# Optimization experiments

Measured on AMD Instinct MI355X. Metric: run time of the kernel, lower is better.

## Reference

```python
import jax, jax.numpy as jnp
import numpy as np

B, N, DIM = 2, 2048, 512
H = 8
DH = DIM // H
ALPHA = 1.0
DELTA = 1.0
EPS = 1e-5


def setup_inputs() -> dict:
    key = jax.random.key(0)
    ks = jax.random.split(key, 5)
    scale = 0.02
    return {
        "z": jax.random.normal(ks[0], (B, N, DIM), dtype=jnp.float32),
        "Wq": jax.random.normal(ks[1], (DIM, DIM), dtype=jnp.float32) * scale,
        "bq": jnp.zeros((DIM,), dtype=jnp.float32),
        "Wk": jax.random.normal(ks[2], (DIM, DIM), dtype=jnp.float32) * scale,
        "bk": jnp.zeros((DIM,), dtype=jnp.float32),
        "Wv": jax.random.normal(ks[3], (DIM, DIM), dtype=jnp.float32) * scale,
        "bv": jnp.zeros((DIM,), dtype=jnp.float32),
        "Wo": jax.random.normal(ks[4], (DIM, DIM), dtype=jnp.float32) * scale,
        "bo": jnp.zeros((DIM,), dtype=jnp.float32),
    }


def _split_heads(x):
    # [B, N, DIM] -> [B, H, N, DH]
    b, n, _ = x.shape
    return x.reshape(b, n, H, DH).transpose(0, 2, 1, 3)


def reference(z, Wq, bq, Wk, bk, Wv, bv, Wo, bo):
    Q = _split_heads(z @ Wq + bq)
    K = _split_heads(z @ Wk + bk)
    V = _split_heads(z @ Wv + bv)

    # QK^T once; reuse for both the score and the squared-distance expansion
    qk = jnp.einsum("bhnd,bhmd->bhnm", Q, K)  # [B,H,N,N]

    # NeuroFocal deviation NF(Q): per-query scalar
    mu_q = Q.mean(axis=-1, keepdims=True)
    var_q = ((Q - mu_q) ** 2).mean(axis=-1, keepdims=True)
    sigma_q = jnp.sqrt(var_q + EPS)
    nf_q = jnp.abs(Q - mu_q).sum(axis=-1, keepdims=True) / (sigma_q + EPS)  # [B,H,N,1]

    # ||Q - K||^2 = |Q|^2 + |K|^2 - 2 QK^T (same math as explicit diff tensor)
    q2 = (Q ** 2).sum(axis=-1)  # [B,H,N]
    k2 = (K ** 2).sum(axis=-1)  # [B,H,N]
    omega = q2[..., :, None] + k2[..., None, :] - 2.0 * qk  # [B,H,N,N]
    omega = omega / (jnp.exp(-DELTA * nf_q) + 1.0)

    logits = qk / jnp.sqrt(jnp.float32(DH)) - ALPHA * omega
    A = jax.nn.softmax(logits, axis=-1)

    out = jnp.einsum("bhnm,bhmd->bhnd", A, V)  # [B,H,N,DH]
    out = out.transpose(0, 2, 1, 3).reshape(z.shape[0], z.shape[1], DIM)
    return out @ Wo + bo
```

## Files before the change

kernel.cpp:

```cpp
#include <hip/hip_runtime.h>
#include <hip/hip_bf16.h>

#define HH 8
#define NNq 2048
#define EPSF 1e-5f
#define LOG2E 1.4426950408889634f

typedef __bf16 bf16x8 __attribute__((ext_vector_type(8)));
typedef float f32x4 __attribute__((ext_vector_type(4)));

typedef const __attribute__((address_space(1))) unsigned int* gas_t;
typedef __attribute__((address_space(3))) unsigned int* las_t;

__device__ __forceinline__ void async16(const void* g, void* l) {
  __builtin_amdgcn_global_load_lds((gas_t)g, (las_t)l, 16, 0, 0);
}
__device__ __forceinline__ void async4(const void* g, void* l) {
  __builtin_amdgcn_global_load_lds((gas_t)g, (las_t)l, 4, 0, 0);
}

__device__ __forceinline__ unsigned short f2bf(float f) {
  union { float f; unsigned int u; } a;
  a.f = f;
  unsigned int r = a.u + 0x7fffu + ((a.u >> 16) & 1u);
  return (unsigned short)(r >> 16);
}

__device__ __forceinline__ int swzk(int row, int k) {
  return (k & ~63) | ((((k >> 3) ^ row) & 7) << 3) | (k & 7);
}

__global__ __launch_bounds__(256) void prep_kernel(
    const float* __restrict__ z, const float* __restrict__ W0,
    const float* __restrict__ W1, const float* __restrict__ W2,
    const float* __restrict__ W3, unsigned short* __restrict__ zb,
    unsigned short* __restrict__ Wt, unsigned int* __restrict__ k2max) {
  __shared__ float Tl[64][68];
  const int t = threadIdx.x;
  const int bx = blockIdx.x;
  if (bx < 1024) {
    const int i = (bx * 256 + t) * 8;
    const int row = i >> 9, k = i & 511;
    const float4 a = *(const float4*)&z[i];
    const float4 b = *(const float4*)&z[i + 4];
    union { unsigned short us[8]; uint4 v; } o;
    o.us[0] = f2bf(a.x); o.us[1] = f2bf(a.y); o.us[2] = f2bf(a.z); o.us[3] = f2bf(a.w);
    o.us[4] = f2bf(b.x); o.us[5] = f2bf(b.y); o.us[6] = f2bf(b.z); o.us[7] = f2bf(b.w);
    *(uint4*)&zb[(row << 9) | swzk(row, k)] = o.v;
  } else if (bx < 1280) {
    const int idx0 = bx - 1024;
    const int wsel = idx0 >> 6, rem = idx0 & 63;
    const int k0 = (rem >> 3) * 64, n0 = (rem & 7) * 64;
    const float* W = (wsel == 0) ? W0 : (wsel == 1) ? W1 : (wsel == 2) ? W2 : W3;
    unsigned short* dst = Wt + (size_t)wsel * 262144;
#pragma unroll
    for (int i = 0; i < 4; ++i) {
      const int idx = t + 256 * i;
      const int row = idx >> 4, cq = (idx & 15) * 4;
      *(float4*)&Tl[row][cq] = *(const float4*)&W[(size_t)(k0 + row) * 512 + n0 + cq];
    }
    __syncthreads();
#pragma unroll
    for (int i = 0; i < 4; ++i) {
      const int idx = t + 256 * i;
      const int nr = idx >> 4, kq = (idx & 15) * 4;
      ushort4 o;
      o.x = f2bf(Tl[kq + 0][nr]);
      o.y = f2bf(Tl[kq + 1][nr]);
      o.z = f2bf(Tl[kq + 2][nr]);
      o.w = f2bf(Tl[kq + 3][nr]);
      const int n = n0 + nr;
      *(ushort4*)&dst[(size_t)n * 512 + swzk(n, k0 + kq)] = o;
    }
  } else {
    k2max[t] = 0u;
  }
}

__global__ __launch_bounds__(256) void gemm_qkv(
    const unsigned short* __restrict__ A, const unsigned short* __restrict__ Wt3,
    const float* __restrict__ bq, const float* __restrict__ bk,
    const float* __restrict__ bvv, unsigned short* __restrict__ Qb,
    unsigned short* __restrict__ Ksw, unsigned short* __restrict__ Vsw,
    float* __restrict__ c1a, float* __restrict__ dva, float* __restrict__ k2a,
    float* __restrict__ q2a, unsigned int* __restrict__ k2max) {
  __shared__ __align__(16) unsigned short S[24576];
  __shared__ float wmax[4];

  const int which = blockIdx.z;
  const unsigned short* Wt = Wt3 + (size_t)which * 262144;
  const float* bias = (which == 0) ? bq : (which == 1) ? bk : bvv;

  const int t = threadIdx.x;
  const int w = t >> 6, lane = t & 63, ln = lane & 15, quad = lane >> 4;
  const int r0 = blockIdx.x * 128, h = blockIdx.y;
  const int c0 = h * 64;
  const int b = r0 >> 11, n0 = r0 & 2047;
  const int bh = b * HH + h;

  f32x4 acc[2][4];
#pragma unroll
  for (int rf = 0; rf < 2; ++rf)
#pragma unroll
    for (int nt = 0; nt < 4; ++nt) acc[rf][nt] = (f32x4)(0.0f);

  const int lr = lane >> 4, lc = (lane & 15) * 8;

  for (int k0 = 0; k0 < 512; k0 += 128) {
#pragma unroll
    for (int i = 0; i < 8; ++i)
      async16(A + (size_t)(r0 + w * 32 + i * 4 + lr) * 512 + k0 + lc,
              S + (w * 32 + i * 4) * 128);
#pragma unroll
    for (int i = 0; i < 4; ++i)
      async16(Wt + (size_t)(c0 + w * 16 + i * 4 + lr) * 512 + k0 + lc,
              S + 16384 + (w * 16 + i * 4) * 128);
    __syncthreads();
#pragma unroll
    for (int kk = 0; kk < 128; kk += 32) {
      const int cp = (kk >> 3) + quad;
      const int cs = ((cp & 8) | ((cp ^ (ln & 7)) & 7)) * 8;
      bf16x8 af[2];
#pragma unroll
      for (int rf = 0; rf < 2; ++rf)
        af[rf] = *(const bf16x8*)&S[(w * 32 + rf * 16 + ln) * 128 + cs];
#pragma unroll
      for (int nt = 0; nt < 4; ++nt) {
        const bf16x8 bf = *(const bf16x8*)&S[16384 + (nt * 16 + ln) * 128 + cs];
#pragma unroll
        for (int rf = 0; rf < 2; ++rf)
          acc[rf][nt] = __builtin_amdgcn_mfma_f32_16x16x32_bf16(af[rf], bf, acc[rf][nt], 0, 0, 0);
      }
    }
    __syncthreads();
  }

  float x[2][4][4];
#pragma unroll
  for (int nt = 0; nt < 4; ++nt) {
    const float bv = bias[c0 + nt * 16 + ln];
#pragma unroll
    for (int rf = 0; rf < 2; ++rf)
#pragma unroll
      for (int r = 0; r < 4; ++r) x[rf][nt][r] = acc[rf][nt][r] + bv;
  }

  if (which == 0) {
#pragma unroll
    for (int rf = 0; rf < 2; ++rf)
#pragma unroll
      for (int r = 0; r < 4; ++r) {
        float s1 = x[rf][0][r] + x[rf][1][r] + x[rf][2][r] + x[rf][3][r];
#pragma unroll
        for (int off = 1; off < 16; off <<= 1) s1 += __shfl_xor(s1, off, 64);
        const float mu = s1 * (1.0f / 64.0f);
        float s2 = 0.0f, sa = 0.0f;
#pragma unroll
        for (int nt = 0; nt < 4; ++nt) {
          const float dx = x[rf][nt][r] - mu;
          s2 += dx * dx;
          sa += fabsf(dx);
        }
#pragma unroll
        for (int off = 1; off < 16; off <<= 1) {
          s2 += __shfl_xor(s2, off, 64);
          sa += __shfl_xor(sa, off, 64);
        }
        if (ln == 0) {
          const float sigma = sqrtf(s2 * (1.0f / 64.0f) + EPSF);
          const float nf = sa / (sigma + EPSF);
          const float dInv = 1.0f / (__expf(-nf) + 1.0f);
          const int row = bh * NNq + n0 + w * 32 + rf * 16 + quad * 4 + r;
          c1a[row] = (0.125f + 2.0f * dInv) * LOG2E;
          dva[row] = dInv * LOG2E;
          q2a[row] = s2 + 64.0f * mu * mu;
        }
      }
#pragma unroll
    for (int rf = 0; rf < 2; ++rf)
#pragma unroll
      for (int nt = 0; nt < 4; ++nt)
#pragma unroll
        for (int r = 0; r < 4; ++r)
          S[(w * 32 + rf * 16 + quad * 4 + r) * 72 + nt * 16 + ln] = f2bf(x[rf][nt][r]);
    __syncthreads();
#pragma unroll
    for (int i = 0; i < 4; ++i) {
      const int idx = t + 256 * i;
      const int q = idx >> 3, c = idx & 7;
      *(uint4*)&Qb[((size_t)bh * NNq + n0 + q) * 64 + c * 8] =
          *(const uint4*)&S[q * 72 + c * 8];
    }
  } else if (which == 1) {
    float mx = 0.0f;
#pragma unroll
    for (int rf = 0; rf < 2; ++rf)
#pragma unroll
      for (int r = 0; r < 4; ++r) {
        float s2 = 0.0f;
#pragma unroll
        for (int nt = 0; nt < 4; ++nt) s2 += x[rf][nt][r] * x[rf][nt][r];
#pragma unroll
        for (int off = 1; off < 16; off <<= 1) s2 += __shfl_xor(s2, off, 64);
        if (ln == 0) k2a[bh * NNq + n0 + w * 32 + rf * 16 + quad * 4 + r] = s2;
        mx = fmaxf(mx, s2);
      }
#pragma unroll
    for (int off = 16; off < 64; off <<= 1) mx = fmaxf(mx, __shfl_xor(mx, off, 64));
    if (lane == 0) wmax[w] = mx;
#pragma unroll
    for (int rf = 0; rf < 2; ++rf)
#pragma unroll
      for (int nt = 0; nt < 4; ++nt) {
        const int c = nt * 2 + (ln >> 3);
#pragma unroll
        for (int r = 0; r < 4; ++r) {
          const int key = w * 32 + rf * 16 + quad * 4 + r;
          const int klo = key & 63;
          S[(key >> 6) * 4096 + klo * 64 + ((c ^ (klo & 7)) * 8) + (ln & 7)] =
              f2bf(x[rf][nt][r]);
        }
      }
    __syncthreads();
    if (t == 0) {
      const float m = fmaxf(fmaxf(wmax[0], wmax[1]), fmaxf(wmax[2], wmax[3]));
      atomicMax(&k2max[bh * 16], __float_as_uint(m));
    }
    unsigned short* dst = Ksw + ((size_t)bh * 32 + (n0 >> 6)) * 4096;
#pragma unroll
    for (int i = 0; i < 4; ++i) {
      const int idx = t + 256 * i;
      *(uint4*)&dst[idx * 8] = *(const uint4*)&S[idx * 8];
    }
  } else {
#pragma unroll
    for (int rf = 0; rf < 2; ++rf)
#pragma unroll
      for (int nt = 0; nt < 4; ++nt) {
        const int d = nt * 16 + ln;
#pragma unroll
        for (int r = 0; r < 4; ++r) {
          const int key = w * 32 + rf * 16 + quad * 4 + r;
          const int klo = key & 63;
          S[d * 128 + (key >> 6) * 64 + (((klo >> 3) ^ (d & 7)) * 8) + (klo & 7)] =
              f2bf(x[rf][nt][r]);
        }
      }
    __syncthreads();
    unsigned short* dst = Vsw + ((size_t)bh * 32 + (n0 >> 6)) * 4096;
#pragma unroll
    for (int i = 0; i < 4; ++i) {
      const int g = t + 256 * i;
      const int tile = g >> 9, d = (g >> 3) & 63, j8 = (g & 7) * 8;
      *(uint4*)&dst[tile * 4096 + d * 64 + j8] =
          *(const uint4*)&S[d * 128 + tile * 64 + j8];
    }
  }
}

__global__ __launch_bounds__(512) void attn_kernel(
    const unsigned short* __restrict__ Qb, const unsigned short* __restrict__ Ksw,
    const unsigned short* __restrict__ Vsw, const float* __restrict__ c1a,
    const float* __restrict__ dva, const float* __restrict__ k2a,
    const float* __restrict__ q2a, const unsigned int* __restrict__ k2maxu,
    unsigned short* __restrict__ attnb) {
  __shared__ __align__(16) char smem[59392];

  const int t = threadIdx.x;
  const int w8 = t >> 6, lane = t & 63, ln = lane & 15, quad = lane >> 4;
  const int half = w8 >> 2, wl = w8 & 3;
  const int qt = blockIdx.x, bh = blockIdx.y;
  const int b = bh >> 3, h = bh & 7;
  const int q0 = qt * 64;
  const int rowbase = bh * NNq;

  unsigned short* Kt = (unsigned short*)(smem + half * 16384);
  unsigned short* Vt = (unsigned short*)(smem + half * 16384 + 8192);
  unsigned short* Ps = (unsigned short*)(smem + 32768 + half * 9216);
  float* k2h = (float*)(smem + 51200 + half * 4096);

  const float* k2g = k2a + rowbase + half * 1024;
#pragma unroll
  for (int i = 0; i < 4; ++i)
    async4(k2g + wl * 256 + i * 64 + lane, k2h + wl * 256 + i * 64);

  const int qg = q0 + wl * 16 + ln;
  const unsigned short* qrow = Qb + ((size_t)rowbase + qg) * 64;
  const bf16x8 aq0 = *(const bf16x8*)(qrow + quad * 8);
  const bf16x8 aq1 = *(const bf16x8*)(qrow + 32 + quad * 8);

  const float k2m = __uint_as_float(k2maxu[bh * 16]);
  const float c1q = c1a[rowbase + qg];
  const float dvq = dva[rowbase + qg];
  const float Mqq = c1q * sqrtf(q2a[rowbase + qg] * k2m);
  float L = 0.0f;
  f32x4 O[4];
#pragma unroll
  for (int nt = 0; nt < 4; ++nt) O[nt] = (f32x4)(0.0f);

  const unsigned short* Kg = Ksw + (size_t)bh * 32 * 4096;
  const unsigned short* Vg = Vsw + (size_t)bh * 32 * 4096;
  const int sw = quad ^ (ln & 7);
  const int sw1 = (4 + quad) ^ (ln & 7);

  for (int kt = 0; kt < 16; ++kt) {
    {
      const size_t tb = (size_t)(half * 16 + kt) * 4096 + wl * 1024;
      async16(Kg + tb + lane * 8, Kt + wl * 1024);
      async16(Kg + tb + 512 + lane * 8, Kt + wl * 1024 + 512);
      async16(Vg + tb + lane * 8, Vt + wl * 1024);
      async16(Vg + tb + 512 + lane * 8, Vt + wl * 1024 + 512);
    }
    __syncthreads();

    f32x4 s[4];
#pragma unroll
    for (int nt = 0; nt < 4; ++nt) {
      const unsigned short* kb = Kt + (nt * 16 + ln) * 64;
      const bf16x8 b0 = *(const bf16x8*)(kb + sw * 8);
      const bf16x8 b1 = *(const bf16x8*)(kb + sw1 * 8);
      f32x4 a = (f32x4)(0.0f);
      a = __builtin_amdgcn_mfma_f32_16x16x32_bf16(b0, aq0, a, 0, 0, 0);
      a = __builtin_amdgcn_mfma_f32_16x16x32_bf16(b1, aq1, a, 0, 0, 0);
      s[nt] = a;
    }

#pragma unroll
    for (int nt = 0; nt < 4; ++nt) {
      const f32x4 k2v = *(const f32x4*)&k2h[kt * 64 + nt * 16 + quad * 4];
      const float p0 = __builtin_amdgcn_exp2f(c1q * s[nt][0] - dvq * k2v[0] - Mqq);
      const float p1 = __builtin_amdgcn_exp2f(c1q * s[nt][1] - dvq * k2v[1] - Mqq);
      const float p2 = __builtin_amdgcn_exp2f(c1q * s[nt][2] - dvq * k2v[2] - Mqq);
      const float p3 = __builtin_amdgcn_exp2f(c1q * s[nt][3] - dvq * k2v[3] - Mqq);
      L += (p0 + p1) + (p2 + p3);
      union { __hip_bfloat162 h; unsigned int u; } c01, c23;
      c01.h = __float22bfloat162_rn(make_float2(p0, p1));
      c23.h = __float22bfloat162_rn(make_float2(p2, p3));
      uint2 pu; pu.x = c01.u; pu.y = c23.u;
      *(uint2*)&Ps[(wl * 16 + ln) * 72 + nt * 16 + quad * 4] = pu;
    }
    const unsigned short* pr = Ps + (wl * 16 + ln) * 72;
    const bf16x8 pa0 = *(const bf16x8*)(pr + quad * 8);
    const bf16x8 pa1 = *(const bf16x8*)(pr + 32 + quad * 8);

#pragma unroll
    for (int nt = 0; nt < 4; ++nt) {
      const unsigned short* vb = Vt + (nt * 16 + ln) * 64;
      const bf16x8 vb0 = *(const bf16x8*)(vb + sw * 8);
      const bf16x8 vb1 = *(const bf16x8*)(vb + sw1 * 8);
      O[nt] = __builtin_amdgcn_mfma_f32_16x16x32_bf16(pa0, vb0, O[nt], 0, 0, 0);
      O[nt] = __builtin_amdgcn_mfma_f32_16x16x32_bf16(pa1, vb1, O[nt], 0, 0, 0);
    }
    __syncthreads();
  }

  L += __shfl_xor(L, 16, 64);
  L += __shfl_xor(L, 32, 64);

  float* Ost = (float*)(smem + half * 16384);
  float* Lst = (float*)(smem + 32768 + half * 9216);
#pragma unroll
  for (int nt = 0; nt < 4; ++nt)
#pragma unroll
    for (int r = 0; r < 4; ++r)
      Ost[(wl * 16 + quad * 4 + r) * 64 + nt * 16 + ln] = O[nt][r];
  if (quad == 0) Lst[wl * 16 + ln] = L;
  __syncthreads();

  const float* O0 = (const float*)smem;
  const float* O1 = (const float*)(smem + 16384);
  const float* L0 = (const float*)(smem + 32768);
  const float* L1 = (const float*)(smem + 32768 + 9216);
  const int q = t >> 3, c8 = (t & 7) * 8;
  const float inv = 1.0f / (L0[q] + L1[q]);
  const int base = q * 64 + c8;
  float4 a0 = *(const float4*)&O0[base];
  float4 a1 = *(const float4*)&O0[base + 4];
  const float4 b0 = *(const float4*)&O1[base];
  const float4 b1 = *(const float4*)&O1[base + 4];
  union { unsigned short us[8]; uint4 v; } ov;
  ov.us[0] = f2bf((a0.x + b0.x) * inv);
  ov.us[1] = f2bf((a0.y + b0.y) * inv);
  ov.us[2] = f2bf((a0.z + b0.z) * inv);
  ov.us[3] = f2bf((a0.w + b0.w) * inv);
  ov.us[4] = f2bf((a1.x + b1.x) * inv);
  ov.us[5] = f2bf((a1.y + b1.y) * inv);
  ov.us[6] = f2bf((a1.z + b1.z) * inv);
  ov.us[7] = f2bf((a1.w + b1.w) * inv);
  const int nrow = q0 + q;
  *(uint4*)&attnb[((size_t)(b * NNq + nrow)) * 512 + swzk(nrow, h * 64 + c8)] = ov.v;
}

__global__ __launch_bounds__(256) void gemm_out(
    const unsigned short* __restrict__ A, const unsigned short* __restrict__ Wt,
    const float* __restrict__ bias, float* __restrict__ of) {
  __shared__ __align__(16) char sbuf[32768];
  unsigned short* S = (unsigned short*)sbuf;
  float (*Tl)[68] = (float(*)[68])sbuf;

  const int t = threadIdx.x;
  const int w = t >> 6, lane = t & 63, ln = lane & 15, quad = lane >> 4;
  const int r0 = blockIdx.x * 64, c0 = blockIdx.y * 64;
  const int lr = lane >> 4, lc = (lane & 15) * 8;

  f32x4 acc[4];
#pragma unroll
  for (int nt = 0; nt < 4; ++nt) acc[nt] = (f32x4)(0.0f);

  for (int k0 = 0; k0 < 512; k0 += 128) {
#pragma unroll
    for (int i = 0; i < 4; ++i) {
      async16(A + (size_t)(r0 + w * 16 + i * 4 + lr) * 512 + k0 + lc,
              S + (w * 16 + i * 4) * 128);
      async16(Wt + (size_t)(c0 + w * 16 + i * 4 + lr) * 512 + k0 + lc,
              S + 8192 + (w * 16 + i * 4) * 128);
    }
    __syncthreads();
#pragma unroll
    for (int kk = 0; kk < 128; kk += 32) {
      const int cp = (kk >> 3) + quad;
      const int cs = ((cp & 8) | ((cp ^ (ln & 7)) & 7)) * 8;
      const bf16x8 af = *(const bf16x8*)&S[(w * 16 + ln) * 128 + cs];
#pragma unroll
      for (int nt = 0; nt < 4; ++nt) {
        const bf16x8 bf = *(const bf16x8*)&S[8192 + (nt * 16 + ln) * 128 + cs];
        acc[nt] = __builtin_amdgcn_mfma_f32_16x16x32_bf16(af, bf, acc[nt], 0, 0, 0);
      }
    }
    __syncthreads();
  }
#pragma unroll
  for (int nt = 0; nt < 4; ++nt) {
    const float bv = bias[c0 + nt * 16 + ln];
#pragma unroll
    for (int r = 0; r < 4; ++r)
      Tl[w * 16 + quad * 4 + r][nt * 16 + ln] = acc[nt][r] + bv;
  }
  __syncthreads();
#pragma unroll
  for (int i = 0; i < 4; ++i) {
    const int idx = t + 256 * i;
    const int row = idx >> 4, c4 = (idx & 15) * 4;
    *(float4*)&of[(size_t)(r0 + row) * 512 + c0 + c4] = *(const float4*)&Tl[row][c4];
  }
}

extern "C" void kernel_launch(void* const* d_in, const int* in_sizes, int n_in,
                              void* d_out, int out_size, void* d_ws,
                              size_t ws_size, hipStream_t stream) {
  const float* z = (const float*)d_in[0];
  const float* Wq = (const float*)d_in[1];
  const float* bq = (const float*)d_in[2];
  const float* Wk = (const float*)d_in[3];
  const float* bk = (const float*)d_in[4];
  const float* Wv = (const float*)d_in[5];
  const float* bv = (const float*)d_in[6];
  const float* Wo = (const float*)d_in[7];
  const float* bo = (const float*)d_in[8];
  float* out = (float*)d_out;

  char* ws = (char*)d_ws;
  unsigned short* zb = (unsigned short*)(ws);
  unsigned short* Wt = (unsigned short*)(ws + 4194304);
  unsigned short* Qb = (unsigned short*)(ws + 6291456);
  unsigned short* Ksw = (unsigned short*)(ws + 10485760);
  unsigned short* Vsw = (unsigned short*)(ws + 14680064);
  float* c1 = (float*)(ws + 18874368);
  float* dv = (float*)(ws + 19005440);
  float* k2 = (float*)(ws + 19136512);
  float* q2 = (float*)(ws + 19267584);
  unsigned short* attnb = (unsigned short*)(ws + 19398656);
  unsigned int* k2max = (unsigned int*)(ws + 23592960);

  hipLaunchKernelGGL(prep_kernel, dim3(1281), dim3(256), 0, stream, z, Wq, Wk,
                     Wv, Wo, zb, Wt, k2max);
  hipLaunchKernelGGL(gemm_qkv, dim3(32, 8, 3), dim3(256), 0, stream, zb, Wt,
                     bq, bk, bv, Qb, Ksw, Vsw, c1, dv, k2, q2, k2max);
  hipLaunchKernelGGL(attn_kernel, dim3(32, 16), dim3(512), 0, stream, Qb, Ksw,
                     Vsw, c1, dv, k2, q2, k2max, attnb);
  hipLaunchKernelGGL(gemm_out, dim3(64, 8), dim3(256), 0, stream, attnb,
                     Wt + 786432, bo, out);
}
```

Baseline: 135.3 us.

## Split attention over key chunks with 32x32 MFMA and separate combine kernel

The attention kernel now splits each query tile's keys into four chunks across a third grid dimension, giving 2048 blocks of 256 threads instead of 512 blocks of 512. Each block writes unnormalized partial O and L to a workspace, and a new combine kernel sums the partials, normalizes and writes bf16 output. The inner loop also moves from 16x16x32 to 32x32x16 MFMA tiles, with a 2x2 wave split over queries and keys. This is meant to raise occupancy and parallelism on a small problem, at the cost of an extra launch and fp32 partial traffic through global memory (about 32 MB).

```diff
diff --git a/kernel.cpp b/kernel.cpp
--- a/kernel.cpp
+++ b/kernel.cpp
@@ -8,6 +8,7 @@
 
 typedef __bf16 bf16x8 __attribute__((ext_vector_type(8)));
 typedef float f32x4 __attribute__((ext_vector_type(4)));
+typedef float f32x16 __attribute__((ext_vector_type(16)));
 
 typedef const __attribute__((address_space(1))) unsigned int* gas_t;
 typedef __attribute__((address_space(3))) unsigned int* las_t;
@@ -258,137 +259,171 @@
   }
 }
 
-__global__ __launch_bounds__(512) void attn_kernel(
+__global__ __launch_bounds__(256) void attn_kernel(
     const unsigned short* __restrict__ Qb, const unsigned short* __restrict__ Ksw,
     const unsigned short* __restrict__ Vsw, const float* __restrict__ c1a,
     const float* __restrict__ dva, const float* __restrict__ k2a,
     const float* __restrict__ q2a, const unsigned int* __restrict__ k2maxu,
-    unsigned short* __restrict__ attnb) {
-  __shared__ __align__(16) char smem[59392];
+    float* __restrict__ Opart, float* __restrict__ Lpart) {
+  __shared__ __align__(16) char smem[28672];
+  unsigned short* Kt = (unsigned short*)smem;
+  unsigned short* Vt = (unsigned short*)(smem + 8192);
+  float* k2h = (float*)(smem + 26624);
 
   const int t = threadIdx.x;
-  const int w8 = t >> 6, lane = t & 63, ln = lane & 15, quad = lane >> 4;
-  const int half = w8 >> 2, wl = w8 & 3;
-  const int qt = blockIdx.x, bh = blockIdx.y;
-  const int b = bh >> 3, h = bh & 7;
+  const int w4 = t >> 6, lane = t & 63, lq = lane & 31, lh = lane >> 5;
+  const int qi = w4 & 1, ki = w4 >> 1;
+  const int qt = blockIdx.x, bh = blockIdx.y, ks = blockIdx.z;
   const int q0 = qt * 64;
   const int rowbase = bh * NNq;
-
-  unsigned short* Kt = (unsigned short*)(smem + half * 16384);
-  unsigned short* Vt = (unsigned short*)(smem + half * 16384 + 8192);
-  unsigned short* Ps = (unsigned short*)(smem + 32768 + half * 9216);
-  float* k2h = (float*)(smem + 51200 + half * 4096);
-
-  const float* k2g = k2a + rowbase + half * 1024;
-#pragma unroll
-  for (int i = 0; i < 4; ++i)
-    async4(k2g + wl * 256 + i * 64 + lane, k2h + wl * 256 + i * 64);
-
-  const int qg = q0 + wl * 16 + ln;
+  const int pb = (qt * 16 + bh) * 4 + ks;
+
+  unsigned short* Ps = (unsigned short*)(smem + 16384 + w4 * 2560);
+
+  const float* k2g = k2a + rowbase + ks * 512;
+  async4(k2g + (w4 * 2 + 0) * 64 + lane, k2h + (w4 * 2 + 0) * 64);
+  async4(k2g + (w4 * 2 + 1) * 64 + lane, k2h + (w4 * 2 + 1) * 64);
+
+  const int qg = q0 + qi * 32 + lq;
   const unsigned short* qrow = Qb + ((size_t)rowbase + qg) * 64;
-  const bf16x8 aq0 = *(const bf16x8*)(qrow + quad * 8);
-  const bf16x8 aq1 = *(const bf16x8*)(qrow + 32 + quad * 8);
+  bf16x8 bq[4];
+#pragma unroll
+  for (int T = 0; T < 4; ++T) bq[T] = *(const bf16x8*)(qrow + T * 16 + lh * 8);
 
   const float k2m = __uint_as_float(k2maxu[bh * 16]);
   const float c1q = c1a[rowbase + qg];
   const float dvq = dva[rowbase + qg];
   const float Mqq = c1q * sqrtf(q2a[rowbase + qg] * k2m);
   float L = 0.0f;
-  f32x4 O[4];
-#pragma unroll
-  for (int nt = 0; nt < 4; ++nt) O[nt] = (f32x4)(0.0f);
-
-  const unsigned short* Kg = Ksw + (size_t)bh * 32 * 4096;
-  const unsigned short* Vg = Vsw + (size_t)bh * 32 * 4096;
-  const int sw = quad ^ (ln & 7);
-  const int sw1 = (4 + quad) ^ (ln & 7);
-
-  for (int kt = 0; kt < 16; ++kt) {
+  f32x16 O[2];
+  O[0] = (f32x16)(0.0f);
+  O[1] = (f32x16)(0.0f);
+
+  const unsigned short* Kg = Ksw + ((size_t)bh * 32 + ks * 8) * 4096;
+  const unsigned short* Vg = Vsw + ((size_t)bh * 32 + ks * 8) * 4096;
+  const int krow = ki * 32 + lq;
+
+  for (int kt = 0; kt < 8; ++kt) {
     {
-      const size_t tb = (size_t)(half * 16 + kt) * 4096 + wl * 1024;
-      async16(Kg + tb + lane * 8, Kt + wl * 1024);
-      async16(Kg + tb + 512 + lane * 8, Kt + wl * 1024 + 512);
-      async16(Vg + tb + lane * 8, Vt + wl * 1024);
-      async16(Vg + tb + 512 + lane * 8, Vt + wl * 1024 + 512);
-    }
-    __syncthreads();
-
-    f32x4 s[4];
-#pragma unroll
-    for (int nt = 0; nt < 4; ++nt) {
-      const unsigned short* kb = Kt + (nt * 16 + ln) * 64;
-      const bf16x8 b0 = *(const bf16x8*)(kb + sw * 8);
-      const bf16x8 b1 = *(const bf16x8*)(kb + sw1 * 8);
-      f32x4 a = (f32x4)(0.0f);
-      a = __builtin_amdgcn_mfma_f32_16x16x32_bf16(b0, aq0, a, 0, 0, 0);
-      a = __builtin_amdgcn_mfma_f32_16x16x32_bf16(b1, aq1, a, 0, 0, 0);
-      s[nt] = a;
-    }
-
-#pragma unroll
-    for (int nt = 0; nt < 4; ++nt) {
-      const f32x4 k2v = *(const f32x4*)&k2h[kt * 64 + nt * 16 + quad * 4];
-      const float p0 = __builtin_amdgcn_exp2f(c1q * s[nt][0] - dvq * k2v[0] - Mqq);
-      const float p1 = __builtin_amdgcn_exp2f(c1q * s[nt][1] - dvq * k2v[1] - Mqq);
-      const float p2 = __builtin_amdgcn_exp2f(c1q * s[nt][2] - dvq * k2v[2] - Mqq);
-      const float p3 = __builtin_amdgcn_exp2f(c1q * s[nt][3] - dvq * k2v[3] - Mqq);
+      const size_t tb = (size_t)kt * 4096 + w4 * 1024;
+      async16(Kg + tb + lane * 8, Kt + w4 * 1024);
+      async16(Kg + tb + 512 + lane * 8, Kt + w4 * 1024 + 512);
+      async16(Vg + tb + lane * 8, Vt + w4 * 1024);
+      async16(Vg + tb + 512 + lane * 8, Vt + w4 * 1024 + 512);
+    }
+    __syncthreads();
+
+    f32x16 s = (f32x16)(0.0f);
+    const unsigned short* kb = Kt + krow * 64;
+#pragma unroll
+    for (int T = 0; T < 4; ++T) {
+      const int chunk = (T * 2 + lh) ^ (krow & 7);
+      const bf16x8 ak = *(const bf16x8*)(kb + chunk * 8);
+      s = __builtin_amdgcn_mfma_f32_32x32x16_bf16(ak, bq[T], s, 0, 0, 0);
+    }
+
+#pragma unroll
+    for (int rq = 0; rq < 4; ++rq) {
+      const int kb4 = 4 * lh + 8 * rq;
+      const f32x4 k2v = *(const f32x4*)&k2h[kt * 64 + ki * 32 + kb4];
+      const float p0 = __builtin_amdgcn_exp2f(c1q * s[rq * 4 + 0] - dvq * k2v[0] - Mqq);
+      const float p1 = __builtin_amdgcn_exp2f(c1q * s[rq * 4 + 1] - dvq * k2v[1] - Mqq);
+      const float p2 = __builtin_amdgcn_exp2f(c1q * s[rq * 4 + 2] - dvq * k2v[2] - Mqq);
+      const float p3 = __builtin_amdgcn_exp2f(c1q * s[rq * 4 + 3] - dvq * k2v[3] - Mqq);
       L += (p0 + p1) + (p2 + p3);
       union { __hip_bfloat162 h; unsigned int u; } c01, c23;
       c01.h = __float22bfloat162_rn(make_float2(p0, p1));
       c23.h = __float22bfloat162_rn(make_float2(p2, p3));
       uint2 pu; pu.x = c01.u; pu.y = c23.u;
-      *(uint2*)&Ps[(wl * 16 + ln) * 72 + nt * 16 + quad * 4] = pu;
-    }
-    const unsigned short* pr = Ps + (wl * 16 + ln) * 72;
-    const bf16x8 pa0 = *(const bf16x8*)(pr + quad * 8);
-    const bf16x8 pa1 = *(const bf16x8*)(pr + 32 + quad * 8);
-
-#pragma unroll
-    for (int nt = 0; nt < 4; ++nt) {
-      const unsigned short* vb = Vt + (nt * 16 + ln) * 64;
-      const bf16x8 vb0 = *(const bf16x8*)(vb + sw * 8);
-      const bf16x8 vb1 = *(const bf16x8*)(vb + sw1 * 8);
-      O[nt] = __builtin_amdgcn_mfma_f32_16x16x32_bf16(pa0, vb0, O[nt], 0, 0, 0);
-      O[nt] = __builtin_amdgcn_mfma_f32_16x16x32_bf16(pa1, vb1, O[nt], 0, 0, 0);
-    }
-    __syncthreads();
-  }
-
-  L += __shfl_xor(L, 16, 64);
+      *(uint2*)&Ps[lq * 40 + kb4] = pu;
+    }
+
+    bf16x8 pa[2];
+#pragma unroll
+    for (int T2 = 0; T2 < 2; ++T2)
+      pa[T2] = *(const bf16x8*)&Ps[lq * 40 + T2 * 16 + lh * 8];
+#pragma unroll
+    for (int dt = 0; dt < 2; ++dt) {
+      const int dcol = dt * 32 + lq;
+      const unsigned short* vb = Vt + dcol * 64;
+#pragma unroll
+      for (int T2 = 0; T2 < 2; ++T2) {
+        const int chunk = (ki * 4 + T2 * 2 + lh) ^ (dcol & 7);
+        const bf16x8 bv = *(const bf16x8*)(vb + chunk * 8);
+        O[dt] = __builtin_amdgcn_mfma_f32_32x32x16_bf16(pa[T2], bv, O[dt], 0, 0, 0);
+      }
+    }
+    __syncthreads();
+  }
+
   L += __shfl_xor(L, 32, 64);
 
-  float* Ost = (float*)(smem + half * 16384);
-  float* Lst = (float*)(smem + 32768 + half * 9216);
-#pragma unroll
-  for (int nt = 0; nt < 4; ++nt)
-#pragma unroll
-    for (int r = 0; r < 4; ++r)
-      Ost[(wl * 16 + quad * 4 + r) * 64 + nt * 16 + ln] = O[nt][r];
-  if (quad == 0) Lst[wl * 16 + ln] = L;
+  float* Ost = (float*)smem;
+  float* Lst = (float*)(smem + 16384);
+  if (ki == 0) {
+#pragma unroll
+    for (int dt = 0; dt < 2; ++dt)
+#pragma unroll
+      for (int r = 0; r < 16; ++r) {
+        const int qrow2 = qi * 32 + (r & 3) + 8 * (r >> 2) + 4 * lh;
+        Ost[qrow2 * 64 + dt * 32 + lq] = O[dt][r];
+      }
+    if (lane < 32) Lst[qi * 32 + lq] = L;
+  }
   __syncthreads();
-
-  const float* O0 = (const float*)smem;
-  const float* O1 = (const float*)(smem + 16384);
-  const float* L0 = (const float*)(smem + 32768);
-  const float* L1 = (const float*)(smem + 32768 + 9216);
-  const int q = t >> 3, c8 = (t & 7) * 8;
-  const float inv = 1.0f / (L0[q] + L1[q]);
-  const int base = q * 64 + c8;
-  float4 a0 = *(const float4*)&O0[base];
-  float4 a1 = *(const float4*)&O0[base + 4];
-  const float4 b0 = *(const float4*)&O1[base];
-  const float4 b1 = *(const float4*)&O1[base + 4];
-  union { unsigned short us[8]; uint4 v; } ov;
-  ov.us[0] = f2bf((a0.x + b0.x) * inv);
-  ov.us[1] = f2bf((a0.y + b0.y) * inv);
-  ov.us[2] = f2bf((a0.z + b0.z) * inv);
-  ov.us[3] = f2bf((a0.w + b0.w) * inv);
-  ov.us[4] = f2bf((a1.x + b1.x) * inv);
-  ov.us[5] = f2bf((a1.y + b1.y) * inv);
-  ov.us[6] = f2bf((a1.z + b1.z) * inv);
-  ov.us[7] = f2bf((a1.w + b1.w) * inv);
-  const int nrow = q0 + q;
-  *(uint4*)&attnb[((size_t)(b * NNq + nrow)) * 512 + swzk(nrow, h * 64 + c8)] = ov.v;
+  if (ki == 1) {
+#pragma unroll
+    for (int dt = 0; dt < 2; ++dt)
+#pragma unroll
+      for (int r = 0; r < 16; ++r) {
+        const int qrow2 = qi * 32 + (r & 3) + 8 * (r >> 2) + 4 * lh;
+        Ost[qrow2 * 64 + dt * 32 + lq] += O[dt][r];
+      }
+    if (lane < 32) Lst[qi * 32 + lq] += L;
+  }
+  __syncthreads();
+#pragma unroll
+  for (int i = 0; i < 4; ++i) {
+    const int f4 = t + i * 256;
+    *(float4*)&Opart[(size_t)pb * 4096 + f4 * 4] = *(const float4*)&Ost[f4 * 4];
+  }
+  if (t < 64) Lpart[pb * 64 + t] = Lst[t];
+}
+
+__global__ __launch_bounds__(256) void attn_combine(
+    const float* __restrict__ Opart, const float* __restrict__ Lpart,
+    unsigned short* __restrict__ attnb) {
+  const int t = threadIdx.x;
+  const int qt = blockIdx.x, bh = blockIdx.y;
+  const int b = bh >> 3, h = bh & 7;
+  const int q = t >> 2, dseg = (t & 3) * 16;
+  const int pbase = (qt * 16 + bh) * 4;
+
+  float Ls = 0.0f;
+#pragma unroll
+  for (int ks = 0; ks < 4; ++ks) Ls += Lpart[(pbase + ks) * 64 + q];
+  const float inv = 1.0f / Ls;
+
+  float acc[16];
+#pragma unroll
+  for (int j = 0; j < 16; ++j) acc[j] = 0.0f;
+#pragma unroll
+  for (int ks = 0; ks < 4; ++ks) {
+    const float* src = Opart + (size_t)(pbase + ks) * 4096 + q * 64 + dseg;
+#pragma unroll
+    for (int i = 0; i < 4; ++i) {
+      const float4 v = *(const float4*)&src[i * 4];
+      acc[i * 4 + 0] += v.x; acc[i * 4 + 1] += v.y;
+      acc[i * 4 + 2] += v.z; acc[i * 4 + 3] += v.w;
+    }
+  }
+  union { unsigned short us[16]; uint4 v[2]; } ov;
+#pragma unroll
+  for (int j = 0; j < 16; ++j) ov.us[j] = f2bf(acc[j] * inv);
+  const int n = qt * 64 + q;
+  unsigned short* dst = attnb + ((size_t)(b * NNq + n)) * 512;
+  *(uint4*)&dst[swzk(n, h * 64 + dseg)] = ov.v[0];
+  *(uint4*)&dst[swzk(n, h * 64 + dseg + 8)] = ov.v[1];
 }
 
 __global__ __launch_bounds__(256) void gemm_out(
@@ -471,13 +506,17 @@
   float* q2 = (float*)(ws + 19267584);
   unsigned short* attnb = (unsigned short*)(ws + 19398656);
   unsigned int* k2max = (unsigned int*)(ws + 23592960);
+  float* Opart = (float*)(ws + 23593984);
+  float* Lpart = (float*)(ws + 57148416);
 
   hipLaunchKernelGGL(prep_kernel, dim3(1281), dim3(256), 0, stream, z, Wq, Wk,
                      Wv, Wo, zb, Wt, k2max);
   hipLaunchKernelGGL(gemm_qkv, dim3(32, 8, 3), dim3(256), 0, stream, zb, Wt,
                      bq, bk, bv, Qb, Ksw, Vsw, c1, dv, k2, q2, k2max);
-  hipLaunchKernelGGL(attn_kernel, dim3(32, 16), dim3(512), 0, stream, Qb, Ksw,
-                     Vsw, c1, dv, k2, q2, k2max, attnb);
+  hipLaunchKernelGGL(attn_kernel, dim3(32, 16, 4), dim3(256), 0, stream, Qb,
+                     Ksw, Vsw, c1, dv, k2, q2, k2max, Opart, Lpart);
+  hipLaunchKernelGGL(attn_combine, dim3(32, 16), dim3(256), 0, stream, Opart,
+                     Lpart, attnb);
   hipLaunchKernelGGL(gemm_out, dim3(64, 8), dim3(256), 0, stream, attnb,
                      Wt + 786432, bo, out);
 }
```

New measurement: 147.1 us. 1.09x slower.

## Shrink GEMM tiles for more blocks and compute softmax row sums via MFMA

Applied to the files above, without the earlier changes.

The QKV projection tile drops from 128 to 64 rows and the output projection tile from 64 to 32 columns, doubling the grid of each kernel to fill more compute units on this small problem. The per-lane scalar accumulation of the softmax denominator in attention is replaced by two extra MFMAs against a ones vector, which also drops the cross-lane shuffles. The trade-offs are less operand reuse per block, more redundant loads of A and W, and a row sum that is now taken over bf16-rounded probabilities rather than fp32 ones.

```diff
diff --git a/kernel.cpp b/kernel.cpp
--- a/kernel.cpp
+++ b/kernel.cpp
@@ -84,7 +84,7 @@
     unsigned short* __restrict__ Ksw, unsigned short* __restrict__ Vsw,
     float* __restrict__ c1a, float* __restrict__ dva, float* __restrict__ k2a,
     float* __restrict__ q2a, unsigned int* __restrict__ k2max) {
-  __shared__ __align__(16) unsigned short S[24576];
+  __shared__ __align__(16) unsigned short S[16384];
   __shared__ float wmax[4];
 
   const int which = blockIdx.z;
@@ -93,99 +93,86 @@
 
   const int t = threadIdx.x;
   const int w = t >> 6, lane = t & 63, ln = lane & 15, quad = lane >> 4;
-  const int r0 = blockIdx.x * 128, h = blockIdx.y;
+  const int r0 = blockIdx.x * 64, h = blockIdx.y;
   const int c0 = h * 64;
   const int b = r0 >> 11, n0 = r0 & 2047;
   const int bh = b * HH + h;
 
-  f32x4 acc[2][4];
-#pragma unroll
-  for (int rf = 0; rf < 2; ++rf)
-#pragma unroll
-    for (int nt = 0; nt < 4; ++nt) acc[rf][nt] = (f32x4)(0.0f);
+  f32x4 acc[4];
+#pragma unroll
+  for (int nt = 0; nt < 4; ++nt) acc[nt] = (f32x4)(0.0f);
 
   const int lr = lane >> 4, lc = (lane & 15) * 8;
 
   for (int k0 = 0; k0 < 512; k0 += 128) {
 #pragma unroll
-    for (int i = 0; i < 8; ++i)
-      async16(A + (size_t)(r0 + w * 32 + i * 4 + lr) * 512 + k0 + lc,
-              S + (w * 32 + i * 4) * 128);
-#pragma unroll
-    for (int i = 0; i < 4; ++i)
+    for (int i = 0; i < 4; ++i) {
+      async16(A + (size_t)(r0 + w * 16 + i * 4 + lr) * 512 + k0 + lc,
+              S + (w * 16 + i * 4) * 128);
       async16(Wt + (size_t)(c0 + w * 16 + i * 4 + lr) * 512 + k0 + lc,
-              S + 16384 + (w * 16 + i * 4) * 128);
+              S + 8192 + (w * 16 + i * 4) * 128);
+    }
     __syncthreads();
 #pragma unroll
     for (int kk = 0; kk < 128; kk += 32) {
       const int cp = (kk >> 3) + quad;
       const int cs = ((cp & 8) | ((cp ^ (ln & 7)) & 7)) * 8;
-      bf16x8 af[2];
-#pragma unroll
-      for (int rf = 0; rf < 2; ++rf)
-        af[rf] = *(const bf16x8*)&S[(w * 32 + rf * 16 + ln) * 128 + cs];
+      const bf16x8 af = *(const bf16x8*)&S[(w * 16 + ln) * 128 + cs];
 #pragma unroll
       for (int nt = 0; nt < 4; ++nt) {
-        const bf16x8 bf = *(const bf16x8*)&S[16384 + (nt * 16 + ln) * 128 + cs];
-#pragma unroll
-        for (int rf = 0; rf < 2; ++rf)
-          acc[rf][nt] = __builtin_amdgcn_mfma_f32_16x16x32_bf16(af[rf], bf, acc[rf][nt], 0, 0, 0);
-      }
-    }
-    __syncthreads();
-  }
-
-  float x[2][4][4];
+        const bf16x8 bf = *(const bf16x8*)&S[8192 + (nt * 16 + ln) * 128 + cs];
+        acc[nt] = __builtin_amdgcn_mfma_f32_16x16x32_bf16(af, bf, acc[nt], 0, 0, 0);
+      }
+    }
+    __syncthreads();
+  }
+
+  float x[4][4];
 #pragma unroll
   for (int nt = 0; nt < 4; ++nt) {
     const float bv = bias[c0 + nt * 16 + ln];
 #pragma unroll
-    for (int rf = 0; rf < 2; ++rf)
-#pragma unroll
-      for (int r = 0; r < 4; ++r) x[rf][nt][r] = acc[rf][nt][r] + bv;
-  }
+    for (int r = 0; r < 4; ++r) x[nt][r] = acc[nt][r] + bv;
+  }
+  const int rowl = w * 16 + quad * 4;
 
   if (which == 0) {
 #pragma unroll
-    for (int rf = 0; rf < 2; ++rf)
-#pragma unroll
-      for (int r = 0; r < 4; ++r) {
-        float s1 = x[rf][0][r] + x[rf][1][r] + x[rf][2][r] + x[rf][3][r];
-#pragma unroll
-        for (int off = 1; off < 16; off <<= 1) s1 += __shfl_xor(s1, off, 64);
-        const float mu = s1 * (1.0f / 64.0f);
-        float s2 = 0.0f, sa = 0.0f;
-#pragma unroll
-        for (int nt = 0; nt < 4; ++nt) {
-          const float dx = x[rf][nt][r] - mu;
-          s2 += dx * dx;
-          sa += fabsf(dx);
-        }
-#pragma unroll
-        for (int off = 1; off < 16; off <<= 1) {
-          s2 += __shfl_xor(s2, off, 64);
-          sa += __shfl_xor(sa, off, 64);
-        }
-        if (ln == 0) {
-          const float sigma = sqrtf(s2 * (1.0f / 64.0f) + EPSF);
-          const float nf = sa / (sigma + EPSF);
-          const float dInv = 1.0f / (__expf(-nf) + 1.0f);
-          const int row = bh * NNq + n0 + w * 32 + rf * 16 + quad * 4 + r;
-          c1a[row] = (0.125f + 2.0f * dInv) * LOG2E;
-          dva[row] = dInv * LOG2E;
-          q2a[row] = s2 + 64.0f * mu * mu;
-        }
-      }
-#pragma unroll
-    for (int rf = 0; rf < 2; ++rf)
-#pragma unroll
-      for (int nt = 0; nt < 4; ++nt)
-#pragma unroll
-        for (int r = 0; r < 4; ++r)
-          S[(w * 32 + rf * 16 + quad * 4 + r) * 72 + nt * 16 + ln] = f2bf(x[rf][nt][r]);
-    __syncthreads();
-#pragma unroll
-    for (int i = 0; i < 4; ++i) {
+    for (int r = 0; r < 4; ++r) {
+      float s1 = x[0][r] + x[1][r] + x[2][r] + x[3][r];
+#pragma unroll
+      for (int off = 1; off < 16; off <<= 1) s1 += __shfl_xor(s1, off, 64);
+      const float mu = s1 * (1.0f / 64.0f);
+      float s2 = 0.0f, sa = 0.0f;
+#pragma unroll
+      for (int nt = 0; nt < 4; ++nt) {
+        const float dx = x[nt][r] - mu;
+        s2 += dx * dx;
+        sa += fabsf(dx);
+      }
+#pragma unroll
+      for (int off = 1; off < 16; off <<= 1) {
+        s2 += __shfl_xor(s2, off, 64);
+        sa += __shfl_xor(sa, off, 64);
+      }
+      if (ln == 0) {
+        const float sigma = sqrtf(s2 * (1.0f / 64.0f) + EPSF);
+        const float nf = sa / (sigma + EPSF);
+        const float dInv = 1.0f / (__expf(-nf) + 1.0f);
+        const int row = bh * NNq + n0 + rowl + r;
+        c1a[row] = (0.125f + 2.0f * dInv) * LOG2E;
+        dva[row] = dInv * LOG2E;
+        q2a[row] = s2 + 64.0f * mu * mu;
+      }
+    }
+#pragma unroll
+    for (int nt = 0; nt < 4; ++nt)
+#pragma unroll
+      for (int r = 0; r < 4; ++r)
+        S[(rowl + r) * 72 + nt * 16 + ln] = f2bf(x[nt][r]);
+    __syncthreads();
+#pragma unroll
+    for (int i = 0; i < 2; ++i) {
       const int idx = t + 256 * i;
       const int q = idx >> 3, c = idx & 7;
       *(uint4*)&Qb[((size_t)bh * NNq + n0 + q) * 64 + c * 8] =
@@ -194,33 +181,27 @@
   } else if (which == 1) {
     float mx = 0.0f;
 #pragma unroll
-    for (int rf = 0; rf < 2; ++rf)
-#pragma unroll
-      for (int r = 0; r < 4; ++r) {
-        float s2 = 0.0f;
-#pragma unroll
-        for (int nt = 0; nt < 4; ++nt) s2 += x[rf][nt][r] * x[rf][nt][r];
-#pragma unroll
-        for (int off = 1; off < 16; off <<= 1) s2 += __shfl_xor(s2, off, 64);
-        if (ln == 0) k2a[bh * NNq + n0 + w * 32 + rf * 16 + quad * 4 + r] = s2;
-        mx = fmaxf(mx, s2);
-      }
+    for (int r = 0; r < 4; ++r) {
+      float s2 = 0.0f;
+#pragma unroll
+      for (int nt = 0; nt < 4; ++nt) s2 += x[nt][r] * x[nt][r];
+#pragma unroll
+      for (int off = 1; off < 16; off <<= 1) s2 += __shfl_xor(s2, off, 64);
+      if (ln == 0) k2a[bh * NNq + n0 + rowl + r] = s2;
+      mx = fmaxf(mx, s2);
+    }
 #pragma unroll
     for (int off = 16; off < 64; off <<= 1) mx = fmaxf(mx, __shfl_xor(mx, off, 64));
     if (lane == 0) wmax[w] = mx;
 #pragma unroll
-    for (int rf = 0; rf < 2; ++rf)
-#pragma unroll
-      for (int nt = 0; nt < 4; ++nt) {
-        const int c = nt * 2 + (ln >> 3);
-#pragma unroll
-        for (int r = 0; r < 4; ++r) {
-          const int key = w * 32 + rf * 16 + quad * 4 + r;
-          const int klo = key & 63;
-          S[(key >> 6) * 4096 + klo * 64 + ((c ^ (klo & 7)) * 8) + (ln & 7)] =
-              f2bf(x[rf][nt][r]);
-        }
-      }
+    for (int nt = 0; nt < 4; ++nt) {
+      const int c = nt * 2 + (ln >> 3);
+#pragma unroll
+      for (int r = 0; r < 4; ++r) {
+        const int key = rowl + r;
+        S[key * 64 + ((c ^ (key & 7)) * 8) + (ln & 7)] = f2bf(x[nt][r]);
+      }
+    }
     __syncthreads();
     if (t == 0) {
       const float m = fmaxf(fmaxf(wmax[0], wmax[1]), fmaxf(wmax[2], wmax[3]));
@@ -228,32 +209,26 @@
     }
     unsigned short* dst = Ksw + ((size_t)bh * 32 + (n0 >> 6)) * 4096;
 #pragma unroll
-    for (int i = 0; i < 4; ++i) {
+    for (int i = 0; i < 2; ++i) {
       const int idx = t + 256 * i;
       *(uint4*)&dst[idx * 8] = *(const uint4*)&S[idx * 8];
     }
   } else {
 #pragma unroll
-    for (int rf = 0; rf < 2; ++rf)
-#pragma unroll
-      for (int nt = 0; nt < 4; ++nt) {
-        const int d = nt * 16 + ln;
-#pragma unroll
-        for (int r = 0; r < 4; ++r) {
-          const int key = w * 32 + rf * 16 + quad * 4 + r;
-          const int klo = key & 63;
-          S[d * 128 + (key >> 6) * 64 + (((klo >> 3) ^ (d & 7)) * 8) + (klo & 7)] =
-              f2bf(x[rf][nt][r]);
-        }
-      }
+    for (int nt = 0; nt < 4; ++nt) {
+      const int d = nt * 16 + ln;
+#pragma unroll
+      for (int r = 0; r < 4; ++r) {
+        const int key = rowl + r;
+        S[d * 64 + (((key >> 3) ^ (d & 7)) * 8) + (key & 7)] = f2bf(x[nt][r]);
+      }
+    }
     __syncthreads();
     unsigned short* dst = Vsw + ((size_t)bh * 32 + (n0 >> 6)) * 4096;
 #pragma unroll
-    for (int i = 0; i < 4; ++i) {
-      const int g = t + 256 * i;
-      const int tile = g >> 9, d = (g >> 3) & 63, j8 = (g & 7) * 8;
-      *(uint4*)&dst[tile * 4096 + d * 64 + j8] =
-          *(const uint4*)&S[d * 128 + tile * 64 + j8];
+    for (int i = 0; i < 2; ++i) {
+      const int idx = t + 256 * i;
+      *(uint4*)&dst[idx * 8] = *(const uint4*)&S[idx * 8];
     }
   }
 }
@@ -293,7 +268,11 @@
   const float c1q = c1a[rowbase + qg];
   const float dvq = dva[rowbase + qg];
   const float Mqq = c1q * sqrtf(q2a[rowbase + qg] * k2m);
-  float L = 0.0f;
+
+  const __bf16 onev = (__bf16)1.0f;
+  const bf16x8 ones = {onev, onev, onev, onev, onev, onev, onev, onev};
+
+  f32x4 Lacc = (f32x4)(0.0f);
   f32x4 O[4];
 #pragma unroll
   for (int nt = 0; nt < 4; ++nt) O[nt] = (f32x4)(0.0f);
@@ -332,7 +311,6 @@
       const float p1 = __builtin_amdgcn_exp2f(c1q * s[nt][1] - dvq * k2v[1] - Mqq);
       const float p2 = __builtin_amdgcn_exp2f(c1q * s[nt][2] - dvq * k2v[2] - Mqq);
       const float p3 = __builtin_amdgcn_exp2f(c1q * s[nt][3] - dvq * k2v[3] - Mqq);
-      L += (p0 + p1) + (p2 + p3);
       union { __hip_bfloat162 h; unsigned int u; } c01, c23;
       c01.h = __float22bfloat162_rn(make_float2(p0, p1));
       c23.h = __float22bfloat162_rn(make_float2(p2, p3));
@@ -342,6 +320,9 @@
     const unsigned short* pr = Ps + (wl * 16 + ln) * 72;
     const bf16x8 pa0 = *(const bf16x8*)(pr + quad * 8);
     const bf16x8 pa1 = *(const bf16x8*)(pr + 32 + quad * 8);
+
+    Lacc = __builtin_amdgcn_mfma_f32_16x16x32_bf16(pa0, ones, Lacc, 0, 0, 0);
+    Lacc = __builtin_amdgcn_mfma_f32_16x16x32_bf16(pa1, ones, Lacc, 0, 0, 0);
 
 #pragma unroll
     for (int nt = 0; nt < 4; ++nt) {
@@ -354,9 +335,6 @@
     __syncthreads();
   }
 
-  L += __shfl_xor(L, 16, 64);
-  L += __shfl_xor(L, 32, 64);
-
   float* Ost = (float*)(smem + half * 16384);
   float* Lst = (float*)(smem + 32768 + half * 9216);
 #pragma unroll
@@ -364,7 +342,10 @@
 #pragma unroll
     for (int r = 0; r < 4; ++r)
       Ost[(wl * 16 + quad * 4 + r) * 64 + nt * 16 + ln] = O[nt][r];
-  if (quad == 0) Lst[wl * 16 + ln] = L;
+  if (ln == 0) {
+#pragma unroll
+    for (int r = 0; r < 4; ++r) Lst[wl * 16 + quad * 4 + r] = Lacc[r];
+  }
   __syncthreads();
 
   const float* O0 = (const float*)smem;
@@ -394,27 +375,28 @@
 __global__ __launch_bounds__(256) void gemm_out(
     const unsigned short* __restrict__ A, const unsigned short* __restrict__ Wt,
     const float* __restrict__ bias, float* __restrict__ of) {
-  __shared__ __align__(16) char sbuf[32768];
+  __shared__ __align__(16) char sbuf[24576];
   unsigned short* S = (unsigned short*)sbuf;
-  float (*Tl)[68] = (float(*)[68])sbuf;
+  float (*Tl)[36] = (float(*)[36])sbuf;
 
   const int t = threadIdx.x;
   const int w = t >> 6, lane = t & 63, ln = lane & 15, quad = lane >> 4;
-  const int r0 = blockIdx.x * 64, c0 = blockIdx.y * 64;
+  const int r0 = blockIdx.x * 64, c0 = blockIdx.y * 32;
   const int lr = lane >> 4, lc = (lane & 15) * 8;
 
-  f32x4 acc[4];
-#pragma unroll
-  for (int nt = 0; nt < 4; ++nt) acc[nt] = (f32x4)(0.0f);
+  f32x4 acc[2];
+#pragma unroll
+  for (int nt = 0; nt < 2; ++nt) acc[nt] = (f32x4)(0.0f);
 
   for (int k0 = 0; k0 < 512; k0 += 128) {
 #pragma unroll
-    for (int i = 0; i < 4; ++i) {
+    for (int i = 0; i < 4; ++i)
       async16(A + (size_t)(r0 + w * 16 + i * 4 + lr) * 512 + k0 + lc,
               S + (w * 16 + i * 4) * 128);
-      async16(Wt + (size_t)(c0 + w * 16 + i * 4 + lr) * 512 + k0 + lc,
-              S + 8192 + (w * 16 + i * 4) * 128);
-    }
+#pragma unroll
+    for (int i = 0; i < 2; ++i)
+      async16(Wt + (size_t)(c0 + w * 8 + i * 4 + lr) * 512 + k0 + lc,
+              S + 8192 + (w * 8 + i * 4) * 128);
     __syncthreads();
 #pragma unroll
     for (int kk = 0; kk < 128; kk += 32) {
@@ -422,7 +404,7 @@
       const int cs = ((cp & 8) | ((cp ^ (ln & 7)) & 7)) * 8;
       const bf16x8 af = *(const bf16x8*)&S[(w * 16 + ln) * 128 + cs];
 #pragma unroll
-      for (int nt = 0; nt < 4; ++nt) {
+      for (int nt = 0; nt < 2; ++nt) {
         const bf16x8 bf = *(const bf16x8*)&S[8192 + (nt * 16 + ln) * 128 + cs];
         acc[nt] = __builtin_amdgcn_mfma_f32_16x16x32_bf16(af, bf, acc[nt], 0, 0, 0);
       }
@@ -430,7 +412,7 @@
     __syncthreads();
   }
 #pragma unroll
-  for (int nt = 0; nt < 4; ++nt) {
+  for (int nt = 0; nt < 2; ++nt) {
     const float bv = bias[c0 + nt * 16 + ln];
 #pragma unroll
     for (int r = 0; r < 4; ++r)
@@ -438,9 +420,9 @@
   }
   __syncthreads();
 #pragma unroll
-  for (int i = 0; i < 4; ++i) {
+  for (int i = 0; i < 2; ++i) {
     const int idx = t + 256 * i;
-    const int row = idx >> 4, c4 = (idx & 15) * 4;
+    const int row = idx >> 3, c4 = (idx & 7) * 4;
     *(float4*)&of[(size_t)(r0 + row) * 512 + c0 + c4] = *(const float4*)&Tl[row][c4];
   }
 }
@@ -474,10 +456,10 @@
 
   hipLaunchKernelGGL(prep_kernel, dim3(1281), dim3(256), 0, stream, z, Wq, Wk,
                      Wv, Wo, zb, Wt, k2max);
-  hipLaunchKernelGGL(gemm_qkv, dim3(32, 8, 3), dim3(256), 0, stream, zb, Wt,
+  hipLaunchKernelGGL(gemm_qkv, dim3(64, 8, 3), dim3(256), 0, stream, zb, Wt,
                      bq, bk, bv, Qb, Ksw, Vsw, c1, dv, k2, q2, k2max);
   hipLaunchKernelGGL(attn_kernel, dim3(32, 16), dim3(512), 0, stream, Qb, Ksw,
                      Vsw, c1, dv, k2, q2, k2max, attnb);
-  hipLaunchKernelGGL(gemm_out, dim3(64, 8), dim3(256), 0, stream, attnb,
+  hipLaunchKernelGGL(gemm_out, dim3(64, 16), dim3(256), 0, stream, attnb,
                      Wt + 786432, bo, out);
 }
```

Result: no change. 136.4 us (+0.8%).
